# Optimization experiments

Hardware: AMD Instinct MI355X
Metric: run time of the kernel (lower is better)

The kernel has to match this reference:

```python
import jax, jax.numpy as jnp
import numpy as np

HIDDEN = 4096
N_HEADS = 32
N_KV_HEADS = 8
HEAD_DIM = HIDDEN // N_HEADS  # 128
GROUPS = N_HEADS // N_KV_HEADS  # 4
ROPE_BASE = 10000.0
BATCH, SEQ = 1, 2048


def _rope_cos_sin(position_ids, dim, base):
    # position_ids: [b, s] int -> cos/sin [b, s, dim]
    inv_freq = 1.0 / (base ** (jnp.arange(0, dim, 2, dtype=jnp.float32) / dim))  # [dim/2]
    freqs = position_ids.astype(jnp.float32)[..., None] * inv_freq  # [b, s, dim/2]
    emb = jnp.concatenate([freqs, freqs], axis=-1)  # [b, s, dim]
    return jnp.cos(emb), jnp.sin(emb)


def _rotate_half(x):
    x1, x2 = jnp.split(x, 2, axis=-1)
    return jnp.concatenate([-x2, x1], axis=-1)


def setup_inputs() -> dict:
    key = jax.random.key(0)
    ks = jax.random.split(key, 8)
    s = 0.02
    return {
        'hidden_states': jax.random.normal(ks[0], (BATCH, SEQ, HIDDEN), dtype=jnp.float32),
        'position_ids': jnp.broadcast_to(jnp.arange(SEQ, dtype=jnp.int64), (BATCH, SEQ)),
        'Wq': jax.random.normal(ks[1], (HIDDEN, N_HEADS * HEAD_DIM), dtype=jnp.float32) * s,
        'bq': jax.random.normal(ks[2], (N_HEADS * HEAD_DIM,), dtype=jnp.float32) * s,
        'Wk': jax.random.normal(ks[3], (HIDDEN, N_KV_HEADS * HEAD_DIM), dtype=jnp.float32) * s,
        'bk': jax.random.normal(ks[4], (N_KV_HEADS * HEAD_DIM,), dtype=jnp.float32) * s,
        'Wv': jax.random.normal(ks[5], (HIDDEN, N_KV_HEADS * HEAD_DIM), dtype=jnp.float32) * s,
        'bv': jax.random.normal(ks[6], (N_KV_HEADS * HEAD_DIM,), dtype=jnp.float32) * s,
        'Wo': jax.random.normal(ks[7], (HIDDEN, HIDDEN), dtype=jnp.float32) * s,
    }


def reference(hidden_states, position_ids, Wq, bq, Wk, bk, Wv, bv, Wo):
    b, s, _ = hidden_states.shape
    # QKV projections (bias=True for q/k/v per module)
    q = hidden_states @ Wq + bq  # [b, s, H*d]
    k = hidden_states @ Wk + bk  # [b, s, Hk*d]
    v = hidden_states @ Wv + bv  # [b, s, Hk*d]
    q = q.reshape(b, s, N_HEADS, HEAD_DIM)
    k = k.reshape(b, s, N_KV_HEADS, HEAD_DIM)
    v = v.reshape(b, s, N_KV_HEADS, HEAD_DIM)

    # RoPE gathered by position_ids
    cos, sin = _rope_cos_sin(position_ids, HEAD_DIM, ROPE_BASE)  # [b, s, d]
    cos = cos[:, :, None, :]
    sin = sin[:, :, None, :]
    q = q * cos + _rotate_half(q) * sin
    k = k * cos + _rotate_half(k) * sin

    # GQA causal attention: group query heads over shared kv heads
    qg = q.reshape(b, s, N_KV_HEADS, GROUPS, HEAD_DIM)
    scale = 1.0 / jnp.sqrt(jnp.asarray(HEAD_DIM, dtype=q.dtype))
    scores = jnp.einsum('bqhgd,bkhd->bhgqk', qg, k) * scale  # [b, Hk, g, s, s]
    causal = jnp.tril(jnp.ones((s, s), dtype=bool))
    scores = jnp.where(causal, scores, jnp.finfo(scores.dtype).min)
    probs = jax.nn.softmax(scores, axis=-1)
    out = jnp.einsum('bhgqk,bkhd->bqhgd', probs, v)  # [b, s, Hk, g, d]
    out = out.reshape(b, s, HIDDEN)
    return out @ Wo  # o_proj, bias=False
```

## Files before the change

### kernel.cpp

```cpp
#include <hip/hip_runtime.h>
#include <hip/hip_bf16.h>

typedef __hip_bfloat16 bf16;
typedef __attribute__((ext_vector_type(8))) __bf16 bf16x8;
typedef __attribute__((ext_vector_type(4))) float f32x4;

#define SEQ 2048
#define HID 4096
#define NH 32
#define NKV 8
#define HD 128
#define KVDIM 1024
#define QKVN 6144

#define MiB (1024 * 1024)

__device__ __forceinline__ void gl_lds16(const void* g, void* lds) {
  __builtin_amdgcn_global_load_lds((const __attribute__((address_space(1))) void*)g,
                                   (__attribute__((address_space(3))) void*)lds,
                                   16, 0, 0);
}

__device__ __forceinline__ float unplo(unsigned u) { return __uint_as_float(u << 16); }
__device__ __forceinline__ float unphi(unsigned u) { return __uint_as_float(u & 0xffff0000u); }
__device__ __forceinline__ unsigned packbf(float a, float b) {
  bf16 t[2] = {__float2bfloat16(a), __float2bfloat16(b)};
  return *reinterpret_cast<unsigned*>(t);
}

__global__ void cvt_kernel(const float* __restrict__ in, bf16* __restrict__ out, int n) {
  int i = (blockIdx.x * blockDim.x + threadIdx.x) * 4;
  if (i >= n) return;
  float4 v = *reinterpret_cast<const float4*>(in + i);
  bf16 o[4] = {__float2bfloat16(v.x), __float2bfloat16(v.y),
               __float2bfloat16(v.z), __float2bfloat16(v.w)};
  *reinterpret_cast<short4*>(out + i) = *reinterpret_cast<const short4*>(o);
}

__global__ void concat_bias_kernel(const float* __restrict__ bq, const float* __restrict__ bk,
                                   const float* __restrict__ bv, float* __restrict__ o) {
  int i = blockIdx.x * blockDim.x + threadIdx.x;
  if (i >= QKVN) return;
  o[i] = (i < HID) ? bq[i] : (i < HID + KVDIM ? bk[i - HID] : bv[i - HID - KVDIM]);
}

__global__ void transpose_all_kernel(const float* __restrict__ Wq, const float* __restrict__ Wk,
                                     const float* __restrict__ Wv, const float* __restrict__ Wo,
                                     bf16* __restrict__ Wqkvt, bf16* __restrict__ Wot) {
  __shared__ float tile[32][33];
  int t = blockIdx.x;
  const float* in;
  bf16* out;
  int si, xt, yt;
  if (t < 16384)      { in = Wq; out = Wqkvt;                           si = HID;   xt = t & 127; yt = t >> 7; }
  else if (t < 20480) { t -= 16384; in = Wk; out = Wqkvt + (size_t)HID * HID;           si = KVDIM; xt = t & 31; yt = t >> 5; }
  else if (t < 24576) { t -= 20480; in = Wv; out = Wqkvt + (size_t)(HID + KVDIM) * HID; si = KVDIM; xt = t & 31; yt = t >> 5; }
  else                { t -= 24576; in = Wo; out = Wot;                 si = HID;   xt = t & 127; yt = t >> 7; }
  int c0 = xt * 32, r0 = yt * 32;
  int tx = threadIdx.x, ty = threadIdx.y;
#pragma unroll
  for (int i = 0; i < 32; i += 8)
    tile[ty + i][tx] = in[(size_t)(r0 + ty + i) * si + (c0 + tx)];
  __syncthreads();
#pragma unroll
  for (int i = 0; i < 32; i += 8)
    out[(size_t)(c0 + ty + i) * HID + (r0 + tx)] = __float2bfloat16(tile[tx][ty + i]);
}

__global__ void postqkv_kernel(const bf16* __restrict__ Ch, bf16* __restrict__ Qb,
                               bf16* __restrict__ Kb, bf16* __restrict__ Vt) {
  __shared__ float tile[32][33];
  int b = blockIdx.x;
  int tid = threadIdx.x;
  if (b < 10240) {
    bool isQ = (b < 8192);
    int idx = (isQ ? b : b - 8192) * 256 + tid;
    int j = idx & 31;
    int h = (idx >> 5) & (isQ ? 31 : 7);
    int s = idx >> (isQ ? 10 : 8);
    size_t bi = (size_t)s * QKVN + (isQ ? 0 : HID) + h * HD;
    unsigned u1 = *reinterpret_cast<const unsigned*>(Ch + bi + 2 * j);
    unsigned u2 = *reinterpret_cast<const unsigned*>(Ch + bi + 64 + 2 * j);
    float x1a = unplo(u1), x1b = unphi(u1);
    float x2a = unplo(u2), x2b = unphi(u2);
    float inv0 = __expf(-(float)(2 * j) * 0.14391156831212787f);
    float inv1 = __expf(-(float)(2 * j + 1) * 0.14391156831212787f);
    float sn0, cs0, sn1, cs1;
    __sincosf((float)s * inv0, &sn0, &cs0);
    __sincosf((float)s * inv1, &sn1, &cs1);
    size_t bo = (size_t)s * (isQ ? HID : KVDIM) + h * HD;
    bf16* Ob = isQ ? Qb : Kb;
    *reinterpret_cast<unsigned*>(Ob + bo + 2 * j) =
        packbf(x1a * cs0 - x2a * sn0, x1b * cs1 - x2b * sn1);
    *reinterpret_cast<unsigned*>(Ob + bo + 64 + 2 * j) =
        packbf(x2a * cs0 + x1a * sn0, x2b * cs1 + x1b * sn1);
  } else {
    int t = b - 10240;
    int xt = t & 31, yt = t >> 5;
    int tx = tid & 31, ty = tid >> 5;
#pragma unroll
    for (int i = 0; i < 32; i += 8)
      tile[ty + i][tx] = __bfloat162float(Ch[(size_t)(yt * 32 + ty + i) * QKVN + (HID + KVDIM) + xt * 32 + tx]);
    __syncthreads();
#pragma unroll
    for (int i = 0; i < 32; i += 8)
      Vt[(size_t)(xt * 32 + ty + i) * SEQ + (yt * 32 + tx)] = __float2bfloat16(tile[tx][ty + i]);
  }
}

#define BARRIER() __builtin_amdgcn_s_barrier()
#define LGKM0()                                          \
  {                                                      \
    asm volatile("s_waitcnt lgkmcnt(0)" ::: "memory");   \
    __builtin_amdgcn_sched_barrier(0);                   \
  }
#define MFMA_ACC(d, x, y) d = __builtin_amdgcn_mfma_f32_16x16x32_bf16(x, y, d, 0, 0, 0)

__global__ __launch_bounds__(512, 2) void gemm256_kernel(
    const bf16* __restrict__ A, const bf16* __restrict__ Bt,
    const float* __restrict__ bias, bf16* __restrict__ Ch,
    int N, int Ksub, int lda) {
  __shared__ bf16 lds[2][4][128 * 64];
  const int blk = blockIdx.x;
  const int bx = blk % 24, by = blk / 24;
  const int tid = threadIdx.x;
  const int lane = tid & 63;
  const int w = tid >> 6;
  const int wr = w >> 2, wc = w & 3;
  const int m0 = by * 256;
  const int n0 = bx * 256;
  const bf16* Ab = A;
  const bf16* Btb = Bt;
  const int nt = Ksub >> 6;

#define STAGE(buf, half, t)                                                     \
  {                                                                             \
    const bf16* _s = ((half) < 2) ? Ab : Btb;                                   \
    int _g0 = (((half) < 2) ? m0 : n0) + ((half) & 1) * 128;                    \
    _Pragma("unroll")                                                           \
    for (int _it = 0; _it < 2; ++_it) {                                         \
      int _row = w * 16 + _it * 8 + (lane >> 3);                                \
      int _ch = (lane & 7) ^ (_row & 7);                                        \
      gl_lds16(_s + (size_t)(_g0 + _row) * lda + (size_t)(t) * 64 + _ch * 8,    \
               &lds[buf][half][(w * 16 + _it * 8) * 64]);                       \
    }                                                                           \
  }

  auto rdA = [&](int cur, int mi, int ks) {
    int rr = mi * 16 + (lane & 15);
    int byt = rr * 128 + (((ks * 32 + (lane >> 4) * 8) * 2) ^ ((rr & 7) << 4));
    return *reinterpret_cast<const bf16x8*>(
        reinterpret_cast<const char*>(&lds[cur][wr][0]) + byt);
  };
  auto rdB = [&](int cur, int ni, int ks) {
    int rr = (wc & 1) * 64 + ni * 16 + (lane & 15);
    int byt = rr * 128 + (((ks * 32 + (lane >> 4) * 8) * 2) ^ ((rr & 7) << 4));
    return *reinterpret_cast<const bf16x8*>(
        reinterpret_cast<const char*>(&lds[cur][2 + (wc >> 1)][0]) + byt);
  };

  f32x4 acc[8][4];
  const f32x4 z = {0.f, 0.f, 0.f, 0.f};
#pragma unroll
  for (int i = 0; i < 8; ++i)
#pragma unroll
    for (int j = 0; j < 4; ++j) acc[i][j] = z;

  STAGE(0, 0, 0); STAGE(0, 1, 0); STAGE(0, 2, 0); STAGE(0, 3, 0);
  STAGE(1, 2, 1); STAGE(1, 3, 1); STAGE(1, 0, 1);
  asm volatile("s_waitcnt vmcnt(6)" ::: "memory");
  BARRIER();

  bf16x8 a[4][2], b[4][2];
  int cur = 0;
  for (int t = 0; t < nt; ++t, cur ^= 1) {
#pragma unroll
    for (int mi = 0; mi < 4; ++mi) { a[mi][0] = rdA(cur, mi, 0); a[mi][1] = rdA(cur, mi, 1); }
#pragma unroll
    for (int ni = 0; ni < 2; ++ni) { b[ni][0] = rdB(cur, ni, 0); b[ni][1] = rdB(cur, ni, 1); }
    if (t + 1 < nt) STAGE(cur ^ 1, 1, t + 1);
    BARRIER();
    LGKM0();
    __builtin_amdgcn_s_setprio(1);
#pragma unroll
    for (int mi = 0; mi < 4; ++mi)
#pragma unroll
      for (int ni = 0; ni < 2; ++ni) {
        MFMA_ACC(acc[mi][ni], a[mi][0], b[ni][0]);
        MFMA_ACC(acc[mi][ni], a[mi][1], b[ni][1]);
      }
    __builtin_amdgcn_s_setprio(0);
    BARRIER();
#pragma unroll
    for (int ni = 2; ni < 4; ++ni) { b[ni][0] = rdB(cur, ni, 0); b[ni][1] = rdB(cur, ni, 1); }
    BARRIER();
    LGKM0();
    __builtin_amdgcn_s_setprio(1);
#pragma unroll
    for (int mi = 0; mi < 4; ++mi)
#pragma unroll
      for (int ni = 2; ni < 4; ++ni) {
        MFMA_ACC(acc[mi][ni], a[mi][0], b[ni][0]);
        MFMA_ACC(acc[mi][ni], a[mi][1], b[ni][1]);
      }
    __builtin_amdgcn_s_setprio(0);
    BARRIER();
#pragma unroll
    for (int mi = 0; mi < 4; ++mi) { a[mi][0] = rdA(cur, mi + 4, 0); a[mi][1] = rdA(cur, mi + 4, 1); }
    if (t + 2 < nt) { STAGE(cur, 2, t + 2); STAGE(cur, 3, t + 2); }
    BARRIER();
    LGKM0();
    __builtin_amdgcn_s_setprio(1);
#pragma unroll
    for (int mi = 0; mi < 4; ++mi)
#pragma unroll
      for (int ni = 2; ni < 4; ++ni) {
        MFMA_ACC(acc[mi + 4][ni], a[mi][0], b[ni][0]);
        MFMA_ACC(acc[mi + 4][ni], a[mi][1], b[ni][1]);
      }
    __builtin_amdgcn_s_setprio(0);
    BARRIER();
    if (t + 2 < nt) STAGE(cur, 0, t + 2);
    if (t + 2 < nt) {
      asm volatile("s_waitcnt vmcnt(6)" ::: "memory");
    } else if (t + 1 < nt) {
      asm volatile("s_waitcnt vmcnt(0)" ::: "memory");
    }
    BARRIER();
    __builtin_amdgcn_s_setprio(1);
#pragma unroll
    for (int mi = 0; mi < 4; ++mi)
#pragma unroll
      for (int ni = 0; ni < 2; ++ni) {
        MFMA_ACC(acc[mi + 4][ni], a[mi][0], b[ni][0]);
        MFMA_ACC(acc[mi + 4][ni], a[mi][1], b[ni][1]);
      }
    __builtin_amdgcn_s_setprio(0);
    BARRIER();
  }

#pragma unroll
  for (int ni = 0; ni < 4; ++ni) {
    int col = n0 + wc * 64 + ni * 16 + (lane & 15);
    float bv = bias[col];
#pragma unroll
    for (int mi = 0; mi < 8; ++mi) {
      int rbase = m0 + wr * 128 + mi * 16 + (lane >> 4) * 4;
#pragma unroll
      for (int r = 0; r < 4; ++r)
        Ch[(size_t)(rbase + r) * N + col] = __float2bfloat16(acc[mi][ni][r] + bv);
    }
  }
#undef STAGE
}

__global__ __launch_bounds__(512, 2) void wogemm_kernel(
    const bf16* __restrict__ A,
    const bf16* __restrict__ Bt,
    float* __restrict__ C) {
  __shared__ bf16 lds[2][3][128 * 64];
  const int blk = blockIdx.x;
  const int sw = (blk & 7) * 32 + (blk >> 3);
  const int n0 = (sw & 31) * 128;
  const int m0 = (sw >> 5) * 256;
  const int tid = threadIdx.x;
  const int lane = tid & 63;
  const int w = tid >> 6;
  const int wr = w >> 1, wc = w & 1;
  const int nt = HID / 64;

#define WSTAGE(buf, slot, t)                                                    \
  {                                                                             \
    const bf16* _s = ((slot) == 2) ? Bt : A;                                    \
    int _g0 = ((slot) == 2) ? n0 : (m0 + (slot) * 128);                         \
    _Pragma("unroll")                                                           \
    for (int _it = 0; _it < 2; ++_it) {                                         \
      int _row = w * 16 + _it * 8 + (lane >> 3);                                \
      int _ch = (lane & 7) ^ (_row & 7);                                        \
      gl_lds16(_s + (size_t)(_g0 + _row) * HID + (size_t)(t) * 64 + _ch * 8,    \
               &lds[buf][slot][(w * 16 + _it * 8) * 64]);                       \
    }                                                                           \
  }

  auto rdA = [&](int cur, int mi, int ks) {
    int rr = (wr & 1) * 64 + mi * 16 + (lane & 15);
    int byt = rr * 128 + (((ks * 32 + (lane >> 4) * 8) * 2) ^ ((rr & 7) << 4));
    return *reinterpret_cast<const bf16x8*>(
        reinterpret_cast<const char*>(&lds[cur][wr >> 1][0]) + byt);
  };
  auto rdB = [&](int cur, int ni, int ks) {
    int rr = wc * 64 + ni * 16 + (lane & 15);
    int byt = rr * 128 + (((ks * 32 + (lane >> 4) * 8) * 2) ^ ((rr & 7) << 4));
    return *reinterpret_cast<const bf16x8*>(
        reinterpret_cast<const char*>(&lds[cur][2][0]) + byt);
  };

  f32x4 acc[4][4];
  const f32x4 z = {0.f, 0.f, 0.f, 0.f};
#pragma unroll
  for (int i = 0; i < 4; ++i)
#pragma unroll
    for (int j = 0; j < 4; ++j) acc[i][j] = z;

  WSTAGE(0, 0, 0); WSTAGE(0, 1, 0); WSTAGE(0, 2, 0);
  WSTAGE(1, 2, 1);
  asm volatile("s_waitcnt vmcnt(2)" ::: "memory");
  BARRIER();

  bf16x8 a[2][2], b[4][2];
  int cur = 0;
  for (int t = 0; t < nt; ++t, cur ^= 1) {
#pragma unroll
    for (int mi = 0; mi < 2; ++mi) { a[mi][0] = rdA(cur, mi, 0); a[mi][1] = rdA(cur, mi, 1); }
#pragma unroll
    for (int ni = 0; ni < 4; ++ni) { b[ni][0] = rdB(cur, ni, 0); b[ni][1] = rdB(cur, ni, 1); }
    if (t + 1 < nt) { WSTAGE(cur ^ 1, 0, t + 1); WSTAGE(cur ^ 1, 1, t + 1); }
    LGKM0();
    __builtin_amdgcn_s_setprio(1);
#pragma unroll
    for (int mi = 0; mi < 2; ++mi)
#pragma unroll
      for (int ni = 0; ni < 4; ++ni) {
        MFMA_ACC(acc[mi][ni], a[mi][0], b[ni][0]);
        MFMA_ACC(acc[mi][ni], a[mi][1], b[ni][1]);
      }
    __builtin_amdgcn_s_setprio(0);
    BARRIER();
#pragma unroll
    for (int mi = 0; mi < 2; ++mi) { a[mi][0] = rdA(cur, mi + 2, 0); a[mi][1] = rdA(cur, mi + 2, 1); }
    if (t + 2 < nt) WSTAGE(cur, 2, t + 2);
    LGKM0();
    __builtin_amdgcn_s_setprio(1);
#pragma unroll
    for (int mi = 0; mi < 2; ++mi)
#pragma unroll
      for (int ni = 0; ni < 4; ++ni) {
        MFMA_ACC(acc[mi + 2][ni], a[mi][0], b[ni][0]);
        MFMA_ACC(acc[mi + 2][ni], a[mi][1], b[ni][1]);
      }
    __builtin_amdgcn_s_setprio(0);
    if (t + 1 < nt) {
      if (t + 2 < nt) {
        asm volatile("s_waitcnt vmcnt(2)" ::: "memory");
      } else {
        asm volatile("s_waitcnt vmcnt(0)" ::: "memory");
      }
    }
    BARRIER();
  }

#pragma unroll
  for (int ni = 0; ni < 4; ++ni) {
    int col = n0 + wc * 64 + ni * 16 + (lane & 15);
#pragma unroll
    for (int mi = 0; mi < 4; ++mi) {
      int rbase = m0 + wr * 64 + mi * 16 + (lane >> 4) * 4;
#pragma unroll
      for (int r = 0; r < 4; ++r)
        C[(size_t)(rbase + r) * HID + col] = acc[mi][ni][r];
    }
  }
#undef WSTAGE
}

__global__ __launch_bounds__(256) void attn_kernel(
    const bf16* __restrict__ Q, const bf16* __restrict__ Kb,
    const bf16* __restrict__ Vt, bf16* __restrict__ AO,
    float* __restrict__ Opart, float* __restrict__ Ml) {
  __shared__ bf16 Ks[64 * 128];
  __shared__ bf16 Vs[128 * 64];
  __shared__ bf16 Ps[4][16 * 64];
  const int tid = threadIdx.x, lane = tid & 63, w = tid >> 6;
  const int b = blockIdx.x;
  const int H = b & 31;
  const int tt = b >> 5;
  int qb, lo, hi, half;
  bool split;
  if (tt < 32) {
    qb = 16 + ((31 - tt) >> 1);
    half = tt & 1;
    int n = qb + 1, mid = n >> 1;
    lo = half ? mid : 0;
    hi = half ? n : mid;
    split = true;
  } else {
    qb = 47 - tt;
    half = 0;
    lo = 0;
    hi = qb + 1;
    split = false;
  }
  const int kvh = H >> 2;
  const int qw = qb * 64 + w * 16;
  const int hig = lane >> 4;
  const int q_loc = lane & 15;
  const int qa = qw + q_loc;

  bf16x8 aq[4];
#pragma unroll
  for (int kd = 0; kd < 4; ++kd) {
    int row = qw + q_loc;
    int d = kd * 32 + hig * 8;
    aq[kd] = *reinterpret_cast<const bf16x8*>(Q + (size_t)row * HID + H * HD + d);
  }

  float m_run = -1e30f, l_run = 0.0f;
  f32x4 o[8];
  const f32x4 z = {0.f, 0.f, 0.f, 0.f};
#pragma unroll
  for (int dt = 0; dt < 8; ++dt) o[dt] = z;

  const float scale = 0.08838834764831845f;

  for (int t = lo; t < hi; ++t) {
    int kvbase = t * 64;
#pragma unroll
    for (int it = 0; it < 4; ++it) {
      int c = w * 4 + it;
      int row = c * 4 + (lane >> 4);
      int sb = ((lane & 15) * 16) ^ ((row & 7) << 4);
      gl_lds16(Kb + (size_t)(kvbase + row) * KVDIM + kvh * HD + (sb >> 1), &Ks[c * 512]);
    }
#pragma unroll
    for (int it = 0; it < 4; ++it) {
      int c = w * 4 + it;
      int row = c * 8 + (lane >> 3);
      int sb = ((lane & 7) * 16) ^ ((row & 7) << 4);
      gl_lds16(Vt + (size_t)(kvh * HD + row) * SEQ + kvbase + (sb >> 1), &Vs[c * 512]);
    }
    __syncthreads();

    f32x4 sf[4];
#pragma unroll
    for (int j = 0; j < 4; ++j) sf[j] = z;
#pragma unroll
    for (int j = 0; j < 4; ++j) {
#pragma unroll
      for (int kd = 0; kd < 4; ++kd) {
        int r = j * 16 + q_loc;
        int byt = r * 256 + (((kd * 32 + hig * 8) * 2) ^ ((r & 7) << 4));
        bf16x8 kfr = *reinterpret_cast<const bf16x8*>(reinterpret_cast<const char*>(Ks) + byt);
        sf[j] = __builtin_amdgcn_mfma_f32_16x16x32_bf16(kfr, aq[kd], sf[j], 0, 0, 0);
      }
    }

    float vals[4][4];
    bool diag = (t == qb);
#pragma unroll
    for (int j = 0; j < 4; ++j)
#pragma unroll
      for (int r = 0; r < 4; ++r) {
        float v = sf[j][r] * scale;
        if (diag) {
          int ka = kvbase + j * 16 + hig * 4 + r;
          if (ka > qa) v = -1e30f;
        }
        vals[j][r] = v;
      }

    float m01 = fmaxf(fmaxf(vals[0][0], vals[0][1]), fmaxf(vals[0][2], vals[0][3]));
    float m23 = fmaxf(fmaxf(vals[1][0], vals[1][1]), fmaxf(vals[1][2], vals[1][3]));
    float m45 = fmaxf(fmaxf(vals[2][0], vals[2][1]), fmaxf(vals[2][2], vals[2][3]));
    float m67 = fmaxf(fmaxf(vals[3][0], vals[3][1]), fmaxf(vals[3][2], vals[3][3]));
    float m = fmaxf(fmaxf(m01, m23), fmaxf(m45, m67));
    m = fmaxf(m, __shfl_xor(m, 16));
    m = fmaxf(m, __shfl_xor(m, 32));
    float mn = fmaxf(m_run, m);
    float alpha = __expf(m_run - mn);
    m_run = mn;

    float p[4][4];
    float rs = 0.0f;
#pragma unroll
    for (int j = 0; j < 4; ++j)
#pragma unroll
      for (int r = 0; r < 4; ++r) {
        p[j][r] = __expf(vals[j][r] - mn);
        rs += p[j][r];
      }
    rs += __shfl_xor(rs, 16);
    rs += __shfl_xor(rs, 32);
    l_run = l_run * alpha + rs;

#pragma unroll
    for (int j = 0; j < 4; ++j) {
      bf16 tmp[4] = {__float2bfloat16(p[j][0]), __float2bfloat16(p[j][1]),
                     __float2bfloat16(p[j][2]), __float2bfloat16(p[j][3])};
      int coff = (j * 16 + hig * 4) * 2;
      int byt = q_loc * 128 + (coff ^ ((q_loc & 7) << 4));
      *reinterpret_cast<uint2*>(reinterpret_cast<char*>(&Ps[w][0]) + byt) =
          *reinterpret_cast<const uint2*>(tmp);
    }

#pragma unroll
    for (int r = 0; r < 4; ++r) {
      float alr = __shfl(alpha, hig * 4 + r);
#pragma unroll
      for (int dt = 0; dt < 8; ++dt) o[dt][r] *= alr;
    }

    bf16x8 pa[2];
#pragma unroll
    for (int ks = 0; ks < 2; ++ks) {
      int byt = q_loc * 128 + (((ks * 32 + hig * 8) * 2) ^ ((q_loc & 7) << 4));
      pa[ks] = *reinterpret_cast<const bf16x8*>(reinterpret_cast<const char*>(&Ps[w][0]) + byt);
    }
#pragma unroll
    for (int dt = 0; dt < 8; ++dt)
#pragma unroll
      for (int ks = 0; ks < 2; ++ks) {
        int vrow = dt * 16 + q_loc;
        int byt = vrow * 128 + (((ks * 32 + hig * 8) * 2) ^ ((vrow & 7) << 4));
        bf16x8 vb = *reinterpret_cast<const bf16x8*>(reinterpret_cast<const char*>(Vs) + byt);
        o[dt] = __builtin_amdgcn_mfma_f32_16x16x32_bf16(pa[ks], vb, o[dt], 0, 0, 0);
      }
    __syncthreads();
  }

  if (!split) {
#pragma unroll
    for (int r = 0; r < 4; ++r) {
      float li = __shfl(l_run, hig * 4 + r);
      float linv = 1.0f / li;
#pragma unroll
      for (int dt = 0; dt < 8; ++dt) {
        int qrow = qw + hig * 4 + r;
        int d = dt * 16 + q_loc;
        AO[(size_t)qrow * HID + H * HD + d] = __float2bfloat16(o[dt][r] * linv);
      }
    }
  } else {
    size_t pbase = ((size_t)(half * NH + H) * 1024);
#pragma unroll
    for (int dt = 0; dt < 8; ++dt)
#pragma unroll
      for (int r = 0; r < 4; ++r) {
        int qrow = qw + hig * 4 + r;
        int d = dt * 16 + q_loc;
        Opart[(pbase + (qrow - 1024)) * HD + d] = o[dt][r];
      }
    if (lane < 16) {
      Ml[(pbase + (qa - 1024)) * 2 + 0] = m_run;
      Ml[(pbase + (qa - 1024)) * 2 + 1] = l_run;
    }
  }
}

__global__ __launch_bounds__(256) void merge_kernel(
    const float* __restrict__ Opart, const float* __restrict__ Ml,
    bf16* __restrict__ AO) {
  int i = blockIdx.x * 256 + threadIdx.x;
  int dq = (i & 31) << 2;
  int row = (i >> 5) & 1023;
  int H = i >> 15;
  size_t b1 = (size_t)H * 1024 + row;
  size_t b2 = (size_t)(NH + H) * 1024 + row;
  float m1 = Ml[b1 * 2], l1 = Ml[b1 * 2 + 1];
  float m2 = Ml[b2 * 2], l2 = Ml[b2 * 2 + 1];
  float M = fmaxf(m1, m2);
  float w1 = __expf(m1 - M), w2 = __expf(m2 - M);
  float inv = 1.0f / (l1 * w1 + l2 * w2);
  float4 o1 = *reinterpret_cast<const float4*>(Opart + b1 * HD + dq);
  float4 o2 = *reinterpret_cast<const float4*>(Opart + b2 * HD + dq);
  bf16 o[4] = {__float2bfloat16((o1.x * w1 + o2.x * w2) * inv),
               __float2bfloat16((o1.y * w1 + o2.y * w2) * inv),
               __float2bfloat16((o1.z * w1 + o2.z * w2) * inv),
               __float2bfloat16((o1.w * w1 + o2.w * w2) * inv)};
  *reinterpret_cast<short4*>(AO + (size_t)(1024 + row) * HID + H * HD + dq) =
      *reinterpret_cast<const short4*>(o);
}

extern "C" void kernel_launch(void* const* d_in, const int* in_sizes, int n_in,
                              void* d_out, int out_size, void* d_ws, size_t ws_size,
                              hipStream_t stream) {
  const float* hidden = (const float*)d_in[0];
  const float* Wq = (const float*)d_in[2];
  const float* bq = (const float*)d_in[3];
  const float* Wk = (const float*)d_in[4];
  const float* bk = (const float*)d_in[5];
  const float* Wv = (const float*)d_in[6];
  const float* bv = (const float*)d_in[7];
  const float* Wo = (const float*)d_in[8];
  float* out = (float*)d_out;

  char* ws = (char*)d_ws;
  bf16*  Wqkvt  = (bf16*)(ws + (size_t)0 * MiB);
  bf16*  Xb     = (bf16*)(ws + (size_t)48 * MiB);
  bf16*  Cqkvh  = (bf16*)(ws + (size_t)64 * MiB);
  bf16*  Wot    = (bf16*)(ws + (size_t)88 * MiB);
  bf16*  Qb     = (bf16*)(ws + (size_t)120 * MiB);
  bf16*  Kb     = (bf16*)(ws + (size_t)136 * MiB);
  bf16*  Vt     = (bf16*)(ws + (size_t)140 * MiB);
  float* bqkv   = (float*)Qb;
  bf16*  AO     = Cqkvh;
  float* Opart  = (float*)Wqkvt;
  float* Ml     = (float*)(ws + (size_t)48 * MiB);

  cvt_kernel<<<(SEQ * HID) / 1024, 256, 0, stream>>>(hidden, Xb, SEQ * HID);
  concat_bias_kernel<<<QKVN / 256, 256, 0, stream>>>(bq, bk, bv, bqkv);
  transpose_all_kernel<<<40960, dim3(32, 8), 0, stream>>>(Wq, Wk, Wv, Wo, Wqkvt, Wot);

  gemm256_kernel<<<192, 512, 0, stream>>>(Xb, Wqkvt, bqkv, Cqkvh, QKVN, HID, HID);

  postqkv_kernel<<<12288, 256, 0, stream>>>(Cqkvh, Qb, Kb, Vt);

  attn_kernel<<<1536, 256, 0, stream>>>(Qb, Kb, Vt, AO, Opart, Ml);
  merge_kernel<<<(NH * 1024 * 32) / 256, 256, 0, stream>>>(Opart, Ml, AO);

  wogemm_kernel<<<256, 512, 0, stream>>>(AO, Wot, out);
}
```

Before: 342.2 us.

## Retile QKV GEMM to 256x192 tiles filling all CUs with a two-phase pipeline

The QKV projection GEMM moves from 256x256 tiles (192 blocks) to 256x192 tiles (256 blocks), so the grid matches the 256 CUs on MI355X and avoids leaving CUs idle. The main loop drops from four MFMA phases to two, staging A and B tiles in separate halves with fewer barriers, and block IDs are swizzled for L2 locality. In exchange each block gets less data reuse per tile, and the new vmcnt bookkeeping must stay correct with the changed load counts.

```diff
diff --git a/kernel.cpp b/kernel.cpp
--- a/kernel.cpp
+++ b/kernel.cpp
@@ -116,142 +116,126 @@
   }
 #define MFMA_ACC(d, x, y) d = __builtin_amdgcn_mfma_f32_16x16x32_bf16(x, y, d, 0, 0, 0)
 
-__global__ __launch_bounds__(512, 2) void gemm256_kernel(
-    const bf16* __restrict__ A, const bf16* __restrict__ Bt,
-    const float* __restrict__ bias, bf16* __restrict__ Ch,
-    int N, int Ksub, int lda) {
-  __shared__ bf16 lds[2][4][128 * 64];
+__global__ __launch_bounds__(512, 2) void qkvgemm_kernel(
+    const bf16* __restrict__ A,
+    const bf16* __restrict__ Bt,
+    const float* __restrict__ bias,
+    bf16* __restrict__ Ch) {
+  __shared__ bf16 lds[2][448 * 64];
   const int blk = blockIdx.x;
-  const int bx = blk % 24, by = blk / 24;
+  const int sw = (blk & 7) * 32 + (blk >> 3);
+  const int bx = sw & 31, by = sw >> 5;
+  const int n0 = bx * 192;
+  const int m0 = by * 256;
   const int tid = threadIdx.x;
   const int lane = tid & 63;
   const int w = tid >> 6;
   const int wr = w >> 2, wc = w & 3;
-  const int m0 = by * 256;
-  const int n0 = bx * 256;
-  const bf16* Ab = A;
-  const bf16* Btb = Bt;
-  const int nt = Ksub >> 6;
-
-#define STAGE(buf, half, t)                                                     \
-  {                                                                             \
-    const bf16* _s = ((half) < 2) ? Ab : Btb;                                   \
-    int _g0 = (((half) < 2) ? m0 : n0) + ((half) & 1) * 128;                    \
-    _Pragma("unroll")                                                           \
-    for (int _it = 0; _it < 2; ++_it) {                                         \
-      int _row = w * 16 + _it * 8 + (lane >> 3);                                \
-      int _ch = (lane & 7) ^ (_row & 7);                                        \
-      gl_lds16(_s + (size_t)(_g0 + _row) * lda + (size_t)(t) * 64 + _ch * 8,    \
-               &lds[buf][half][(w * 16 + _it * 8) * 64]);                       \
-    }                                                                           \
+  const int hig = lane >> 4;
+  const int nt = HID / 64;
+
+#define QSTAGE_A(buf, t)                                                          \
+  {                                                                               \
+    _Pragma("unroll")                                                             \
+    for (int _c = 0; _c < 4; ++_c) {                                              \
+      int _row = _c * 64 + w * 8 + (lane >> 3);                                   \
+      int _ch = (lane & 7) ^ ((lane >> 3) & 7);                                   \
+      gl_lds16(A + (size_t)(m0 + _row) * HID + (size_t)(t) * 64 + _ch * 8,        \
+               &lds[buf][(_c * 64 + w * 8) * 64]);                                \
+    }                                                                             \
+  }
+#define QSTAGE_B(buf, t)                                                          \
+  {                                                                               \
+    _Pragma("unroll")                                                             \
+    for (int _c = 0; _c < 3; ++_c) {                                              \
+      int _row = _c * 64 + w * 8 + (lane >> 3);                                   \
+      int _ch = (lane & 7) ^ ((lane >> 3) & 7);                                   \
+      gl_lds16(Bt + (size_t)(n0 + _row) * HID + (size_t)(t) * 64 + _ch * 8,       \
+               &lds[buf][(256 + _c * 64 + w * 8) * 64]);                          \
+    }                                                                             \
   }
 
   auto rdA = [&](int cur, int mi, int ks) {
-    int rr = mi * 16 + (lane & 15);
-    int byt = rr * 128 + (((ks * 32 + (lane >> 4) * 8) * 2) ^ ((rr & 7) << 4));
+    int rr = wr * 128 + mi * 16 + (lane & 15);
+    int byt = rr * 128 + (((ks * 32 + hig * 8) * 2) ^ ((rr & 7) << 4));
     return *reinterpret_cast<const bf16x8*>(
-        reinterpret_cast<const char*>(&lds[cur][wr][0]) + byt);
+        reinterpret_cast<const char*>(&lds[cur][0]) + byt);
   };
   auto rdB = [&](int cur, int ni, int ks) {
-    int rr = (wc & 1) * 64 + ni * 16 + (lane & 15);
-    int byt = rr * 128 + (((ks * 32 + (lane >> 4) * 8) * 2) ^ ((rr & 7) << 4));
+    int rr = wc * 48 + ni * 16 + (lane & 15);
+    int byt = 32768 + rr * 128 + (((ks * 32 + hig * 8) * 2) ^ ((rr & 7) << 4));
     return *reinterpret_cast<const bf16x8*>(
-        reinterpret_cast<const char*>(&lds[cur][2 + (wc >> 1)][0]) + byt);
+        reinterpret_cast<const char*>(&lds[cur][0]) + byt);
   };
 
-  f32x4 acc[8][4];
+  f32x4 acc[8][3];
   const f32x4 z = {0.f, 0.f, 0.f, 0.f};
 #pragma unroll
   for (int i = 0; i < 8; ++i)
 #pragma unroll
-    for (int j = 0; j < 4; ++j) acc[i][j] = z;
-
-  STAGE(0, 0, 0); STAGE(0, 1, 0); STAGE(0, 2, 0); STAGE(0, 3, 0);
-  STAGE(1, 2, 1); STAGE(1, 3, 1); STAGE(1, 0, 1);
-  asm volatile("s_waitcnt vmcnt(6)" ::: "memory");
+    for (int j = 0; j < 3; ++j) acc[i][j] = z;
+
+  QSTAGE_A(0, 0); QSTAGE_B(0, 0);
+  QSTAGE_B(1, 1);
+  asm volatile("s_waitcnt vmcnt(3)" ::: "memory");
   BARRIER();
 
-  bf16x8 a[4][2], b[4][2];
+  bf16x8 a[4][2], b[3][2];
   int cur = 0;
   for (int t = 0; t < nt; ++t, cur ^= 1) {
 #pragma unroll
     for (int mi = 0; mi < 4; ++mi) { a[mi][0] = rdA(cur, mi, 0); a[mi][1] = rdA(cur, mi, 1); }
 #pragma unroll
-    for (int ni = 0; ni < 2; ++ni) { b[ni][0] = rdB(cur, ni, 0); b[ni][1] = rdB(cur, ni, 1); }
-    if (t + 1 < nt) STAGE(cur ^ 1, 1, t + 1);
-    BARRIER();
+    for (int ni = 0; ni < 3; ++ni) { b[ni][0] = rdB(cur, ni, 0); b[ni][1] = rdB(cur, ni, 1); }
+    if (t + 1 < nt) QSTAGE_A(cur ^ 1, t + 1);
     LGKM0();
     __builtin_amdgcn_s_setprio(1);
 #pragma unroll
     for (int mi = 0; mi < 4; ++mi)
 #pragma unroll
-      for (int ni = 0; ni < 2; ++ni) {
+      for (int ni = 0; ni < 3; ++ni) {
         MFMA_ACC(acc[mi][ni], a[mi][0], b[ni][0]);
         MFMA_ACC(acc[mi][ni], a[mi][1], b[ni][1]);
       }
     __builtin_amdgcn_s_setprio(0);
     BARRIER();
 #pragma unroll
-    for (int ni = 2; ni < 4; ++ni) { b[ni][0] = rdB(cur, ni, 0); b[ni][1] = rdB(cur, ni, 1); }
-    BARRIER();
+    for (int mi = 0; mi < 4; ++mi) { a[mi][0] = rdA(cur, mi + 4, 0); a[mi][1] = rdA(cur, mi + 4, 1); }
+    if (t + 2 < nt) QSTAGE_B(cur, t + 2);
     LGKM0();
     __builtin_amdgcn_s_setprio(1);
 #pragma unroll
     for (int mi = 0; mi < 4; ++mi)
 #pragma unroll
-      for (int ni = 2; ni < 4; ++ni) {
-        MFMA_ACC(acc[mi][ni], a[mi][0], b[ni][0]);
-        MFMA_ACC(acc[mi][ni], a[mi][1], b[ni][1]);
-      }
-    __builtin_amdgcn_s_setprio(0);
-    BARRIER();
-#pragma unroll
-    for (int mi = 0; mi < 4; ++mi) { a[mi][0] = rdA(cur, mi + 4, 0); a[mi][1] = rdA(cur, mi + 4, 1); }
-    if (t + 2 < nt) { STAGE(cur, 2, t + 2); STAGE(cur, 3, t + 2); }
-    BARRIER();
-    LGKM0();
-    __builtin_amdgcn_s_setprio(1);
-#pragma unroll
-    for (int mi = 0; mi < 4; ++mi)
-#pragma unroll
-      for (int ni = 2; ni < 4; ++ni) {
+      for (int ni = 0; ni < 3; ++ni) {
         MFMA_ACC(acc[mi + 4][ni], a[mi][0], b[ni][0]);
         MFMA_ACC(acc[mi + 4][ni], a[mi][1], b[ni][1]);
       }
     __builtin_amdgcn_s_setprio(0);
+    if (t + 1 < nt) {
+      if (t + 2 < nt) {
+        asm volatile("s_waitcnt vmcnt(3)" ::: "memory");
+      } else {
+        asm volatile("s_waitcnt vmcnt(0)" ::: "memory");
+      }
+    }
     BARRIER();
-    if (t + 2 < nt) STAGE(cur, 0, t + 2);
-    if (t + 2 < nt) {
-      asm volatile("s_waitcnt vmcnt(6)" ::: "memory");
-    } else if (t + 1 < nt) {
-      asm volatile("s_waitcnt vmcnt(0)" ::: "memory");
-    }
-    BARRIER();
-    __builtin_amdgcn_s_setprio(1);
-#pragma unroll
-    for (int mi = 0; mi < 4; ++mi)
-#pragma unroll
-      for (int ni = 0; ni < 2; ++ni) {
-        MFMA_ACC(acc[mi + 4][ni], a[mi][0], b[ni][0]);
-        MFMA_ACC(acc[mi + 4][ni], a[mi][1], b[ni][1]);
-      }
-    __builtin_amdgcn_s_setprio(0);
-    BARRIER();
-  }
-
-#pragma unroll
-  for (int ni = 0; ni < 4; ++ni) {
-    int col = n0 + wc * 64 + ni * 16 + (lane & 15);
+  }
+
+#pragma unroll
+  for (int ni = 0; ni < 3; ++ni) {
+    int col = n0 + wc * 48 + ni * 16 + (lane & 15);
     float bv = bias[col];
 #pragma unroll
     for (int mi = 0; mi < 8; ++mi) {
-      int rbase = m0 + wr * 128 + mi * 16 + (lane >> 4) * 4;
+      int rbase = m0 + wr * 128 + mi * 16 + hig * 4;
 #pragma unroll
       for (int r = 0; r < 4; ++r)
-        Ch[(size_t)(rbase + r) * N + col] = __float2bfloat16(acc[mi][ni][r] + bv);
-    }
-  }
-#undef STAGE
+        Ch[(size_t)(rbase + r) * QKVN + col] = __float2bfloat16(acc[mi][ni][r] + bv);
+    }
+  }
+#undef QSTAGE_A
+#undef QSTAGE_B
 }
 
 __global__ __launch_bounds__(512, 2) void wogemm_kernel(
@@ -600,7 +584,7 @@
   concat_bias_kernel<<<QKVN / 256, 256, 0, stream>>>(bq, bk, bv, bqkv);
   transpose_all_kernel<<<40960, dim3(32, 8), 0, stream>>>(Wq, Wk, Wv, Wo, Wqkvt, Wot);
 
-  gemm256_kernel<<<192, 512, 0, stream>>>(Xb, Wqkvt, bqkv, Cqkvh, QKVN, HID, HID);
+  qkvgemm_kernel<<<256, 512, 0, stream>>>(Xb, Wqkvt, bqkv, Cqkvh);
 
   postqkv_kernel<<<12288, 256, 0, stream>>>(Cqkvh, Qb, Kb, Vt);
 
```

After: 316.9 us. -7.4%, faster.
